# Kernel optimization log

Measured on AMD Instinct MI355X. Metric: run time of the kernel, lower is better.

Reference implementation:

```python
import jax, jax.numpy as jnp
import numpy as np

N = 32768      # total nodes = 256 graphs x 128 nodes
G = 256        # graphs in batch
NPG = 128      # nodes per graph
DEG = 8        # incoming edges per node
E = N * DEG    # 262144 edges
F_IN = 64      # node feature size
F_E = 16       # edge feature size
EMB = 64       # out_channels per head == embedding_size
H = 4          # attention heads
HC = H * EMB   # 256
DENSE = 256
K = 64         # ceil(0.5 * NPG)
EPS = 1e-5


def setup_inputs() -> dict:
    key = jax.random.key(0)
    ks = list(jax.random.split(key, 32))
    it = iter(ks)
    s = 0.05

    def rn(shape):
        return jax.random.normal(next(it), shape, jnp.float32) * s

    x = jax.random.normal(next(it), (N, F_IN), jnp.float32)
    dst = jnp.repeat(jnp.arange(N, dtype=jnp.int32), DEG)
    src = (dst // NPG) * NPG + jax.random.randint(next(it), (E,), 0, NPG, dtype=jnp.int32)
    edge_index = jnp.stack([src, dst])                      # [2, E], edges stay within graph
    edge_attr = jax.random.normal(next(it), (E, F_E), jnp.float32)
    batch_index = jnp.arange(N, dtype=jnp.int32) // NPG

    inp = dict(
        x=x, edge_index=edge_index, edge_attr=edge_attr, batch_index=batch_index,
        # TransformerConv 1 (in=F_IN)
        Wq1=rn((F_IN, HC)), bq1=jnp.zeros((HC,), jnp.float32),
        Wk1=rn((F_IN, HC)), bk1=jnp.zeros((HC,), jnp.float32),
        Wv1=rn((F_IN, HC)), bv1=jnp.zeros((HC,), jnp.float32),
        We1=rn((F_E, HC)),
        Ws1=rn((F_IN, HC)), bs1=jnp.zeros((HC,), jnp.float32),
        Wb1=rn((3 * HC, 1)),
        t1_W=rn((HC, EMB)), t1_b=jnp.zeros((EMB,), jnp.float32),
        bn1_g=jnp.ones((EMB,), jnp.float32), bn1_b=jnp.zeros((EMB,), jnp.float32),
        # TransformerConv 2 (in=EMB)
        Wq2=rn((EMB, HC)), bq2=jnp.zeros((HC,), jnp.float32),
        Wk2=rn((EMB, HC)), bk2=jnp.zeros((HC,), jnp.float32),
        Wv2=rn((EMB, HC)), bv2=jnp.zeros((HC,), jnp.float32),
        We2=rn((F_E, HC)),
        Ws2=rn((EMB, HC)), bs2=jnp.zeros((HC,), jnp.float32),
        Wb2=rn((3 * HC, 1)),
        t2_W=rn((HC, EMB)), t2_b=jnp.zeros((EMB,), jnp.float32),
        bn2_g=jnp.ones((EMB,), jnp.float32), bn2_b=jnp.zeros((EMB,), jnp.float32),
        # TopKPooling + MLP head
        pool_w=rn((EMB,)),
        l1_W=rn((2 * EMB, DENSE)), l1_b=jnp.zeros((DENSE,), jnp.float32),
        l2_W=rn((DENSE, DENSE // 2)), l2_b=jnp.zeros((DENSE // 2,), jnp.float32),
        l3_W=rn((DENSE // 2, 1)), l3_b=jnp.zeros((1,), jnp.float32),
    )
    return inp


def _tconv(x, src, dst, ea, Wq, bq, Wk, bk, Wv, bv, We, Ws, bs, Wb):
    """PyG TransformerConv with edge_dim, beta=True, concat=True."""
    n = x.shape[0]
    q = (x @ Wq + bq).reshape(n, H, EMB)                    # [N,H,C]
    eemb = (ea @ We).reshape(-1, H, EMB)                    # [E,H,C]
    k = (x @ Wk + bk)[src].reshape(-1, H, EMB) + eemb       # edge features added to key
    v = (x @ Wv + bv)[src].reshape(-1, H, EMB) + eemb       # and to value
    alpha = jnp.einsum('ehc,ehc->eh', q[dst], k) / jnp.sqrt(jnp.float32(EMB))  # [E,H]
    # stable segment softmax over incoming edges of each dst node
    amax = jax.ops.segment_max(alpha, dst, num_segments=n)
    pexp = jnp.exp(alpha - amax[dst])
    denom = jax.ops.segment_sum(pexp, dst, num_segments=n)
    attn = pexp / denom[dst]                                # [E,H]
    out = jax.ops.segment_sum(v * attn[..., None], dst, num_segments=n).reshape(n, HC)
    # beta gated skip: lin_skip(x) and lin_beta([out, xr, out-xr])
    xr = x @ Ws + bs
    beta = jax.nn.sigmoid(jnp.concatenate([out, xr, out - xr], axis=-1) @ Wb)  # [N,1]
    return beta * xr + (1.0 - beta) * out


def _bn(x, g, b):
    m = x.mean(0)
    v = x.var(0)
    return g * (x - m) * jax.lax.rsqrt(v + EPS) + b


def _forward(x, edge_attr,
             Wq1, bq1, Wk1, bk1, Wv1, bv1, We1, Ws1, bs1, Wb1, t1_W, t1_b, bn1_g, bn1_b,
             Wq2, bq2, Wk2, bk2, Wv2, bv2, We2, Ws2, bs2, Wb2, t2_W, t2_b, bn2_g, bn2_b,
             pool_w, l1_W, l1_b, l2_W, l2_b, l3_W, l3_b,
             edge_index, batch_index):
    src, dst = edge_index[0], edge_index[1]
    h = _tconv(x, src, dst, edge_attr, Wq1, bq1, Wk1, bk1, Wv1, bv1, We1, Ws1, bs1, Wb1)
    h = _bn(jax.nn.relu(h @ t1_W + t1_b), bn1_g, bn1_b)
    h = _tconv(h, src, dst, edge_attr, Wq2, bq2, Wk2, bk2, Wv2, bv2, We2, Ws2, bs2, Wb2)
    h = _bn(jax.nn.relu(h @ t2_W + t2_b), bn2_g, bn2_b)
    # TopKPooling: score = (x.w)/||w||, keep top K per graph, scale by tanh(score)
    score = (h @ pool_w) / jnp.linalg.norm(pool_w)          # [N]
    sv, si = jax.lax.top_k(score.reshape(G, NPG), K)        # [G,K]
    xs = jnp.take_along_axis(h.reshape(G, NPG, EMB), si[..., None], axis=1)  # [G,K,EMB]
    xs = xs * jnp.tanh(sv)[..., None]
    # readout: global max pool || global mean pool
    rep = jnp.concatenate([xs.max(axis=1), xs.mean(axis=1)], axis=-1)  # [G, 2*EMB]
    hd = jax.nn.relu(rep @ l1_W + l1_b)
    hd = jax.nn.relu(hd @ l2_W + l2_b)
    return hd @ l3_W + l3_b                                  # [G,1]


def reference(x, edge_index, edge_attr, batch_index,
              Wq1, bq1, Wk1, bk1, Wv1, bv1, We1, Ws1, bs1, Wb1, t1_W, t1_b, bn1_g, bn1_b,
              Wq2, bq2, Wk2, bk2, Wv2, bv2, We2, Ws2, bs2, Wb2, t2_W, t2_b, bn2_g, bn2_b,
              pool_w, l1_W, l1_b, l2_W, l2_b, l3_W, l3_b):
    return _forward(x, edge_attr,
                    Wq1, bq1, Wk1, bk1, Wv1, bv1, We1, Ws1, bs1, Wb1, t1_W, t1_b, bn1_g, bn1_b,
                    Wq2, bq2, Wk2, bk2, Wv2, bv2, We2, Ws2, bs2, Wb2, t2_W, t2_b, bn2_g, bn2_b,
                    pool_w, l1_W, l1_b, l2_W, l2_b, l3_W, l3_b,
                    edge_index, batch_index)
```

## Files before the change

### kernel.cpp

```cpp
#include <hip/hip_runtime.h>
#include <math.h>

#define NN 32768
#define NG 256
#define DEG 8
#define HC 256
#define NCAT 1088
#define HCP 320
#define KTOP 64
#define EPSBN 1e-5f

typedef __attribute__((ext_vector_type(8))) short short8v;
typedef __attribute__((ext_vector_type(4))) float f32x4;

__device__ inline float bf2f(unsigned short u) {
    union { unsigned int i; float f; } c; c.i = ((unsigned int)u) << 16; return c.f;
}
__device__ inline unsigned short f2bf(float f) {
    union { float f; unsigned int i; } c; c.f = f;
    unsigned int r = c.i + 0x7FFFu + ((c.i >> 16) & 1u);
    return (unsigned short)(r >> 16);
}
__device__ inline void split2(float v, unsigned short& hi, unsigned short& lo) {
    hi = f2bf(v);
    lo = f2bf(v - bf2f(hi));
}

__global__ __launch_bounds__(256) void split_x(
    const float* __restrict__ X,
    unsigned short* __restrict__ Xhi, unsigned short* __restrict__ Xlo)
{
    size_t i8 = ((size_t)blockIdx.x * 256 + threadIdx.x) * 8;
    float4 a0 = *(const float4*)(X + i8);
    float4 a1 = *(const float4*)(X + i8 + 4);
    float av[8] = {a0.x, a0.y, a0.z, a0.w, a1.x, a1.y, a1.z, a1.w};
    short8v vh, vl;
    #pragma unroll
    for (int j = 0; j < 8; j++) {
        unsigned short h, l;
        split2(av[j], h, l);
        vh[j] = (short)h; vl[j] = (short)l;
    }
    *(short8v*)(Xhi + i8) = vh;
    *(short8v*)(Xlo + i8) = vl;
}

__global__ __launch_bounds__(256) void prep(
    const float* __restrict__ Wq, const float* __restrict__ bq,
    const float* __restrict__ Wk, const float* __restrict__ bk,
    const float* __restrict__ Wv, const float* __restrict__ bv,
    const float* __restrict__ Ws, const float* __restrict__ bs,
    const float* __restrict__ We, const float* __restrict__ tW,
    const float* __restrict__ Wb,
    unsigned short* __restrict__ WThi, unsigned short* __restrict__ WTlo,
    float* __restrict__ bcat,
    unsigned short* __restrict__ tWThi, unsigned short* __restrict__ tWTlo,
    float* __restrict__ Wbf, float* __restrict__ stats)
{
    const int t = threadIdx.x, b = blockIdx.x;
    if (b < 16) {
        int n = b * 64 + (t >> 2);
        int cc = n & 255;
        const float* src = (n < 256) ? Wq : (n < 512) ? Wk : (n < 768) ? Wv : Ws;
        int k0 = (t & 3) * 16;
        #pragma unroll
        for (int k = k0; k < k0 + 16; k++) {
            unsigned short h, l;
            split2(src[k * 256 + cc], h, l);
            WThi[n * 64 + k] = h; WTlo[n * 64 + k] = l;
        }
    } else if (b < 32) {
        int idx = (b - 16) * 256 + t;
        int k = idx >> 6, o = idx & 63;
        int h = o >> 4, f = o & 15;
        const float* wq = Wq + k * 256 + h * 64;
        const float* we = We + f * 256 + h * 64;
        float s = 0.f;
        #pragma unroll
        for (int d = 0; d < 64; d++) s += wq[d] * we[d];
        unsigned short hh, ll;
        split2(s, hh, ll);
        WThi[(1024 + o) * 64 + k] = hh; WTlo[(1024 + o) * 64 + k] = ll;
    } else if (b < 48) {
        int idx = (b - 32) * 256 + t;
        int kp = idx >> 6, n = idx & 63;
        int h = kp >> 4, f = kp & 15;
        const float* we = We + f * 256 + h * 64;
        const float* tw = tW + (h * 64) * 64 + n;
        float s = 0.f;
        #pragma unroll
        for (int d = 0; d < 64; d++) s += we[d] * tw[d * 64];
        unsigned short hh, ll;
        split2(s, hh, ll);
        tWThi[n * HCP + 256 + kp] = hh; tWTlo[n * HCP + 256 + kp] = ll;
    } else if (b < 64) {
        int base = (b - 48) * 1024 + t * 4;
        #pragma unroll
        for (int i = 0; i < 4; i++) {
            int idx = base + i;
            int n = idx >> 8, k = idx & 255;
            unsigned short h, l;
            split2(tW[k * 64 + n], h, l);
            tWThi[n * HCP + k] = h; tWTlo[n * HCP + k] = l;
        }
    } else {
        if (t < 128) stats[t] = 0.f;
        Wbf[t]       = Wb[t]       + Wb[512 + t];
        Wbf[256 + t] = Wb[256 + t] - Wb[512 + t];
        for (int c = t; c < 1024; c += 256) {
            int cc = c & 255;
            bcat[c] = (c < 256) ? bq[cc] : (c < 512) ? bk[cc] : (c < 768) ? bv[cc] : bs[cc];
        }
        if (t < 64) {
            int h = t >> 4, f = t & 15;
            const float* we = We + f * 256 + h * 64;
            float s = 0.f, sb = 0.f;
            #pragma unroll
            for (int d = 0; d < 64; d++) {
                s  += we[d] * (Wb[h * 64 + d] + Wb[512 + h * 64 + d]);
                sb += we[d] * bq[h * 64 + d];
            }
            Wbf[512 + t] = s;
            bcat[1024 + t] = sb;
        }
    }
}

__global__ __launch_bounds__(256) void proj_mfma(
    const unsigned short* __restrict__ Ahi, const unsigned short* __restrict__ Alo,
    const unsigned short* __restrict__ WThi, const unsigned short* __restrict__ WTlo,
    const float* __restrict__ bcat, unsigned short* __restrict__ C)
{
    __shared__ char smem[32768];
    unsigned short* AhiL = (unsigned short*)smem;
    unsigned short* AloL = AhiL + 4096;
    unsigned short* WhiL = AloL + 4096;
    unsigned short* WloL = WhiL + 4096;
    float* CL = (float*)smem;
    const int t = threadIdx.x;
    const int n0 = blockIdx.x * 64;
    const int row0 = blockIdx.y * 64;

    #pragma unroll
    for (int g = 0; g < 2; g++) {
        int idx = t * 8 + g * 2048;
        int r = idx >> 6, c = idx & 63;
        int ch = (c >> 3) ^ (r & 7);
        *(short8v*)(AhiL + r * 64 + ch * 8) =
            *(const short8v*)(Ahi + (size_t)(row0 + r) * 64 + c);
        *(short8v*)(AloL + r * 64 + ch * 8) =
            *(const short8v*)(Alo + (size_t)(row0 + r) * 64 + c);
        *(short8v*)(WhiL + r * 64 + ch * 8) =
            *(const short8v*)(WThi + (size_t)(n0 + r) * 64 + c);
        *(short8v*)(WloL + r * 64 + ch * 8) =
            *(const short8v*)(WTlo + (size_t)(n0 + r) * 64 + c);
    }
    __syncthreads();

    const int w = t >> 6, l = t & 63;
    const int lr = l & 15, lg = l >> 4, ls = l & 7;
    f32x4 acc[4] = {};
    #pragma unroll
    for (int kk = 0; kk < 2; kk++) {
        int ch = (kk * 4 + lg) ^ ls;
        short8v ah = *(short8v*)(AhiL + (w * 16 + lr) * 64 + ch * 8);
        short8v al = *(short8v*)(AloL + (w * 16 + lr) * 64 + ch * 8);
        #pragma unroll
        for (int nt = 0; nt < 4; nt++) {
            short8v bh = *(short8v*)(WhiL + (nt * 16 + lr) * 64 + ch * 8);
            short8v bl = *(short8v*)(WloL + (nt * 16 + lr) * 64 + ch * 8);
            acc[nt] = __builtin_amdgcn_mfma_f32_16x16x32_bf16(ah, bh, acc[nt], 0, 0, 0);
            acc[nt] = __builtin_amdgcn_mfma_f32_16x16x32_bf16(al, bh, acc[nt], 0, 0, 0);
            acc[nt] = __builtin_amdgcn_mfma_f32_16x16x32_bf16(ah, bl, acc[nt], 0, 0, 0);
        }
    }
    __syncthreads();
    #pragma unroll
    for (int nt = 0; nt < 4; nt++)
        #pragma unroll
        for (int r = 0; r < 4; r++)
            CL[(w * 16 + lg * 4 + r) * 68 + nt * 16 + lr] = acc[nt][r];
    __syncthreads();
    {
        int r = t >> 2, cb = (t & 3) * 16;
        #pragma unroll
        for (int jj = 0; jj < 2; jj++) {
            f32x4 p0 = *(f32x4*)(CL + r * 68 + cb + jj * 8);
            f32x4 p1 = *(f32x4*)(CL + r * 68 + cb + jj * 8 + 4);
            float4 b0 = *(const float4*)(bcat + n0 + cb + jj * 8);
            float4 b1 = *(const float4*)(bcat + n0 + cb + jj * 8 + 4);
            short8v o;
            o[0] = (short)f2bf(p0[0] + b0.x); o[1] = (short)f2bf(p0[1] + b0.y);
            o[2] = (short)f2bf(p0[2] + b0.z); o[3] = (short)f2bf(p0[3] + b0.w);
            o[4] = (short)f2bf(p1[0] + b1.x); o[5] = (short)f2bf(p1[1] + b1.y);
            o[6] = (short)f2bf(p1[2] + b1.z); o[7] = (short)f2bf(p1[3] + b1.w);
            *(short8v*)(C + (size_t)(row0 + r) * NCAT + n0 + cb + jj * 8) = o;
        }
    }
}

__global__ __launch_bounds__(256) void gemm_t(
    const unsigned short* __restrict__ Ahi, const unsigned short* __restrict__ Alo,
    const unsigned short* __restrict__ WThi, const unsigned short* __restrict__ WTlo,
    const float* __restrict__ bias, float* __restrict__ Tout,
    float* __restrict__ stats)
{
    __shared__ char smem[32768];
    unsigned short* AhiL = (unsigned short*)smem;
    unsigned short* AloL = AhiL + 4096;
    unsigned short* WhiL = AloL + 4096;
    unsigned short* WloL = WhiL + 4096;
    float* CL = (float*)smem;
    const int t = threadIdx.x;
    const int row0 = blockIdx.x * 64;
    const int w = t >> 6, l = t & 63;
    const int lr = l & 15, lg = l >> 4, ls = l & 7;
    f32x4 acc[4] = {};
    for (int kt = 0; kt < 5; kt++) {
        if (kt) __syncthreads();
        #pragma unroll
        for (int g = 0; g < 2; g++) {
            int idx = t * 8 + g * 2048;
            int r = idx >> 6, c = idx & 63;
            int ch = (c >> 3) ^ (r & 7);
            *(short8v*)(AhiL + r * 64 + ch * 8) =
                *(const short8v*)(Ahi + (size_t)(row0 + r) * HCP + kt * 64 + c);
            *(short8v*)(AloL + r * 64 + ch * 8) =
                *(const short8v*)(Alo + (size_t)(row0 + r) * HCP + kt * 64 + c);
            *(short8v*)(WhiL + r * 64 + ch * 8) =
                *(const short8v*)(WThi + r * HCP + kt * 64 + c);
            *(short8v*)(WloL + r * 64 + ch * 8) =
                *(const short8v*)(WTlo + r * HCP + kt * 64 + c);
        }
        __syncthreads();
        #pragma unroll
        for (int kk = 0; kk < 2; kk++) {
            int ch = (kk * 4 + lg) ^ ls;
            short8v ah = *(short8v*)(AhiL + (w * 16 + lr) * 64 + ch * 8);
            short8v al = *(short8v*)(AloL + (w * 16 + lr) * 64 + ch * 8);
            #pragma unroll
            for (int nt = 0; nt < 4; nt++) {
                short8v bh = *(short8v*)(WhiL + (nt * 16 + lr) * 64 + ch * 8);
                short8v bl = *(short8v*)(WloL + (nt * 16 + lr) * 64 + ch * 8);
                acc[nt] = __builtin_amdgcn_mfma_f32_16x16x32_bf16(ah, bh, acc[nt], 0, 0, 0);
                acc[nt] = __builtin_amdgcn_mfma_f32_16x16x32_bf16(al, bh, acc[nt], 0, 0, 0);
                acc[nt] = __builtin_amdgcn_mfma_f32_16x16x32_bf16(ah, bl, acc[nt], 0, 0, 0);
            }
        }
    }
    __syncthreads();
    #pragma unroll
    for (int nt = 0; nt < 4; nt++)
        #pragma unroll
        for (int r = 0; r < 4; r++)
            CL[(w * 16 + lg * 4 + r) * 68 + nt * 16 + lr] = acc[nt][r];
    __syncthreads();
    {
        int r = t >> 2, cb = (t & 3) * 16;
        #pragma unroll
        for (int jj = 0; jj < 4; jj++) {
            f32x4 p = *(f32x4*)(CL + r * 68 + cb + jj * 4);
            float4 bb = *(const float4*)(bias + cb + jj * 4);
            float4 o;
            o.x = fmaxf(p[0] + bb.x, 0.f); o.y = fmaxf(p[1] + bb.y, 0.f);
            o.z = fmaxf(p[2] + bb.z, 0.f); o.w = fmaxf(p[3] + bb.w, 0.f);
            *(float4*)(Tout + (size_t)(row0 + r) * 64 + cb + jj * 4) = o;
        }
    }
    if (t < 64) {
        float bb = bias[t];
        float s = 0.f, s2 = 0.f;
        #pragma unroll 8
        for (int r = 0; r < 64; r++) {
            float v = fmaxf(CL[r * 68 + t] + bb, 0.f);
            s += v; s2 += v * v;
        }
        atomicAdd(&stats[t], s);
        atomicAdd(&stats[64 + t], s2);
    }
}

__global__ __launch_bounds__(256) void attn_fused(
    const unsigned short* __restrict__ C,
    const float* __restrict__ Wbf,
    const int* __restrict__ srcIdx, const float* __restrict__ EA,
    unsigned short* __restrict__ Hhi, unsigned short* __restrict__ Hlo)
{
    const int t = threadIdx.x;
    const int lane = t & 63;
    const int bid = blockIdx.x;
    const int swz = (bid & 7) * 512 + (bid >> 3);
    const int n = swz * 8 + (t >> 5);
    const int l = lane & 31;
    const int c0 = l * 8;
    const int h = l >> 3;
    const int fl = l & 7;
    const int gb = lane & 56;

    const unsigned short* rowN = C + (size_t)n * NCAT;
    short8v qv = *(const short8v*)(rowN + c0);
    float q[8];
    #pragma unroll
    for (int i = 0; i < 8; i++) q[i] = bf2f((unsigned short)qv[i]);
    float qe0 = bf2f(rowN[1024 + h * 16 + 2 * fl]);
    float qe1 = bf2f(rowN[1024 + h * 16 + 2 * fl + 1]);

    const int ebase = n * DEG;
    int sj = srcIdx[ebase + fl];
    int ss[DEG];
    #pragma unroll
    for (int j = 0; j < DEG; j++) ss[j] = __shfl(sj, gb | j);

    short8v kv[DEG];
    float2 eav[DEG];
    #pragma unroll
    for (int j = 0; j < DEG; j++) {
        kv[j] = *(const short8v*)(C + (size_t)ss[j] * NCAT + 256 + c0);
        eav[j] = *(const float2*)(EA + (size_t)(ebase + j) * 16 + 2 * fl);
    }
    float alpha[DEG];
    #pragma unroll
    for (int j = 0; j < DEG; j++) {
        float d = eav[j].x * qe0 + eav[j].y * qe1;
        #pragma unroll
        for (int i = 0; i < 8; i++) d += q[i] * bf2f((unsigned short)kv[j][i]);
        alpha[j] = d;
    }
    #pragma unroll
    for (int j = 0; j < DEG; j++) {
        float d = alpha[j];
        d += __shfl_xor(d, 1); d += __shfl_xor(d, 2); d += __shfl_xor(d, 4);
        alpha[j] = d * 0.125f;
    }
    float mx = alpha[0];
    #pragma unroll
    for (int j = 1; j < DEG; j++) mx = fmaxf(mx, alpha[j]);
    float wsum = 0.f, wgt[DEG];
    #pragma unroll
    for (int j = 0; j < DEG; j++) { wgt[j] = expf(alpha[j] - mx); wsum += wgt[j]; }
    float inv = 1.f / wsum;

    float o[8] = {};
    float eg0 = 0.f, eg1 = 0.f;
    #pragma unroll
    for (int j = 0; j < DEG; j++) {
        float wj = wgt[j] * inv;
        eg0 += wj * eav[j].x; eg1 += wj * eav[j].y;
        short8v vv = *(const short8v*)(C + (size_t)ss[j] * NCAT + 512 + c0);
        #pragma unroll
        for (int i = 0; i < 8; i++) o[i] += wj * bf2f((unsigned short)vv[i]);
    }

    short8v sv = *(const short8v*)(rowN + 768 + c0);
    float xr[8];
    #pragma unroll
    for (int i = 0; i < 8; i++) xr[i] = bf2f((unsigned short)sv[i]);

    float2 we13 = *(const float2*)(Wbf + 512 + l * 2);
    float part = eg0 * we13.x + eg1 * we13.y;
    {
        f32x4 w13a = *(const f32x4*)(Wbf + c0);
        f32x4 w13b = *(const f32x4*)(Wbf + c0 + 4);
        f32x4 w23a = *(const f32x4*)(Wbf + 256 + c0);
        f32x4 w23b = *(const f32x4*)(Wbf + 256 + c0 + 4);
        #pragma unroll
        for (int i = 0; i < 4; i++) {
            part += o[i] * w13a[i] + xr[i] * w23a[i];
            part += o[4 + i] * w13b[i] + xr[4 + i] * w23b[i];
        }
    }
    part += __shfl_xor(part, 1);  part += __shfl_xor(part, 2);
    part += __shfl_xor(part, 4);  part += __shfl_xor(part, 8);
    part += __shfl_xor(part, 16);
    float beta = 1.f / (1.f + expf(-part));
    float omb = 1.f - beta;

    short8v hh, hl;
    #pragma unroll
    for (int i = 0; i < 8; i++) {
        float hv = beta * xr[i] + omb * o[i];
        unsigned short a, b;
        split2(hv, a, b);
        hh[i] = (short)a; hl[i] = (short)b;
    }
    *(short8v*)(Hhi + (size_t)n * HCP + c0) = hh;
    *(short8v*)(Hlo + (size_t)n * HCP + c0) = hl;

    ushort2 zh, zl;
    split2(omb * eg0, zh.x, zl.x);
    split2(omb * eg1, zh.y, zl.y);
    *(ushort2*)(Hhi + (size_t)n * HCP + 256 + l * 2) = zh;
    *(ushort2*)(Hlo + (size_t)n * HCP + 256 + l * 2) = zl;
}

__global__ __launch_bounds__(256) void bn_apply(
    float* __restrict__ T, const float* __restrict__ stats,
    const float* __restrict__ g, const float* __restrict__ b,
    unsigned short* __restrict__ Thi, unsigned short* __restrict__ Tlo)
{
    int i = blockIdx.x * 256 + threadIdx.x;
    int c = i & 63;
    float mean = stats[c] * (1.f / NN);
    float var  = stats[64 + c] * (1.f / NN) - mean * mean;
    float v = T[i];
    float r = g[c] * (v - mean) * rsqrtf(var + EPSBN) + b[c];
    T[i] = r;
    unsigned short h, l;
    split2(r, h, l);
    Thi[i] = h; Tlo[i] = l;
}

__global__ __launch_bounds__(128) void pool_mlp(
    const float* __restrict__ Hn, const float* __restrict__ pw,
    const float* __restrict__ W1, const float* __restrict__ b1,
    const float* __restrict__ W2, const float* __restrict__ b2,
    const float* __restrict__ W3, const float* __restrict__ b3,
    float* __restrict__ out)
{
    __shared__ float sh[128][65];
    __shared__ float spw[64];
    __shared__ float sc[128];
    __shared__ float sscale[128];
    __shared__ int   skeep[128];
    __shared__ float rmax[2][64], rsum[2][64];
    __shared__ float srep[128];
    __shared__ float sh1[256];
    __shared__ float sh2[128];
    __shared__ float wred[2];
    const int g = blockIdx.x, t = threadIdx.x;

    for (int i = t; i < 128 * 64; i += 128) sh[i >> 6][i & 63] = Hn[(size_t)g * 128 * 64 + i];
    if (t < 64) spw[t] = pw[t];
    __syncthreads();

    float nw = 0.f;
    #pragma unroll
    for (int i = 0; i < 64; i++) { float w = spw[i]; nw += w * w; }
    float invn = rsqrtf(nw);

    float s = 0.f;
    #pragma unroll
    for (int i = 0; i < 64; i++) s += sh[t][i] * spw[i];
    s *= invn;
    sc[t] = s;
    __syncthreads();

    int rank = 0;
    for (int m = 0; m < 128; m++) {
        float sm = sc[m];
        rank += (sm > s) || (sm == s && m < t);
    }
    skeep[t] = (rank < KTOP);
    sscale[t] = tanhf(s);
    __syncthreads();

    {
        int c = t & 63, half = t >> 6;
        float mxv = -1e30f, sm = 0.f;
        for (int r = half * 64; r < half * 64 + 64; r++) {
            if (skeep[r]) {
                float v = sh[r][c] * sscale[r];
                mxv = fmaxf(mxv, v); sm += v;
            }
        }
        rmax[half][c] = mxv; rsum[half][c] = sm;
    }
    __syncthreads();
    if (t < 64) {
        srep[t] = fmaxf(rmax[0][t], rmax[1][t]);
        srep[64 + t] = (rsum[0][t] + rsum[1][t]) * (1.f / KTOP);
    }
    __syncthreads();

    #pragma unroll
    for (int jj = 0; jj < 2; jj++) {
        int j = t + jj * 128;
        float a = b1[j];
        for (int c2 = 0; c2 < 128; c2++) a += srep[c2] * W1[c2 * 256 + j];
        sh1[j] = fmaxf(a, 0.f);
    }
    __syncthreads();
    {
        float a = b2[t];
        for (int c2 = 0; c2 < 256; c2++) a += sh1[c2] * W2[c2 * 128 + t];
        sh2[t] = fmaxf(a, 0.f);
    }
    __syncthreads();
    float p = sh2[t] * W3[t];
    p += __shfl_xor(p, 1);  p += __shfl_xor(p, 2);  p += __shfl_xor(p, 4);
    p += __shfl_xor(p, 8);  p += __shfl_xor(p, 16); p += __shfl_xor(p, 32);
    if ((t & 63) == 0) wred[t >> 6] = p;
    __syncthreads();
    if (t == 0) out[g] = wred[0] + wred[1] + b3[0];
}

extern "C" void kernel_launch(void* const* d_in, const int* in_sizes, int n_in,
                              void* d_out, int out_size, void* d_ws, size_t ws_size,
                              hipStream_t stream)
{
    const float* x    = (const float*)d_in[0];
    const int*   ei   = (const int*)  d_in[1];
    const float* ea   = (const float*)d_in[2];
    const int*   srcI = ei;
    const float* Wq1 = (const float*)d_in[4];  const float* bq1 = (const float*)d_in[5];
    const float* Wk1 = (const float*)d_in[6];  const float* bk1 = (const float*)d_in[7];
    const float* Wv1 = (const float*)d_in[8];  const float* bv1 = (const float*)d_in[9];
    const float* We1 = (const float*)d_in[10];
    const float* Ws1 = (const float*)d_in[11]; const float* bs1 = (const float*)d_in[12];
    const float* Wb1 = (const float*)d_in[13];
    const float* t1W = (const float*)d_in[14]; const float* t1b = (const float*)d_in[15];
    const float* g1  = (const float*)d_in[16]; const float* be1 = (const float*)d_in[17];
    const float* Wq2 = (const float*)d_in[18]; const float* bq2 = (const float*)d_in[19];
    const float* Wk2 = (const float*)d_in[20]; const float* bk2 = (const float*)d_in[21];
    const float* Wv2 = (const float*)d_in[22]; const float* bv2 = (const float*)d_in[23];
    const float* We2 = (const float*)d_in[24];
    const float* Ws2 = (const float*)d_in[25]; const float* bs2 = (const float*)d_in[26];
    const float* Wb2 = (const float*)d_in[27];
    const float* t2W = (const float*)d_in[28]; const float* t2b = (const float*)d_in[29];
    const float* g2  = (const float*)d_in[30]; const float* be2 = (const float*)d_in[31];
    const float* pw  = (const float*)d_in[32];
    const float* l1W = (const float*)d_in[33]; const float* l1b = (const float*)d_in[34];
    const float* l2W = (const float*)d_in[35]; const float* l2b = (const float*)d_in[36];
    const float* l3W = (const float*)d_in[37]; const float* l3b = (const float*)d_in[38];

    char* ws = (char*)d_ws;
    unsigned short* C   = (unsigned short*)ws;
    unsigned short* Hhi = (unsigned short*)(ws + (size_t)NN * NCAT * 2);
    unsigned short* Hlo = Hhi + (size_t)NN * HCP;
    float* bT    = (float*)(Hlo + (size_t)NN * HCP);
    unsigned short* bThi = (unsigned short*)(bT + (size_t)NN * 64);
    unsigned short* bTlo = bThi + (size_t)NN * 64;
    unsigned short* Xhi  = bTlo + (size_t)NN * 64;
    unsigned short* Xlo  = Xhi + (size_t)NN * 64;
    float* bcat  = (float*)(Xlo + (size_t)NN * 64);
    float* stats = bcat + NCAT;
    float* Wbf   = stats + 128;
    unsigned short* WThi  = (unsigned short*)(Wbf + 576);
    unsigned short* WTlo  = WThi + (size_t)NCAT * 64;
    unsigned short* tWThi = WTlo + (size_t)NCAT * 64;
    unsigned short* tWTlo = tWThi + 64 * HCP;

    const dim3 blk(256);
    const dim3 gProj(17, 512);

    split_x<<<NN * 64 / (256 * 8), blk, 0, stream>>>(x, Xhi, Xlo);
    prep<<<65, blk, 0, stream>>>(Wq1, bq1, Wk1, bk1, Wv1, bv1, Ws1, bs1, We1, t1W, Wb1,
                                 WThi, WTlo, bcat, tWThi, tWTlo, Wbf, stats);
    proj_mfma<<<gProj, blk, 0, stream>>>(Xhi, Xlo, WThi, WTlo, bcat, C);
    attn_fused<<<NN / 8, blk, 0, stream>>>(C, Wbf, srcI, ea, Hhi, Hlo);
    gemm_t<<<512, blk, 0, stream>>>(Hhi, Hlo, tWThi, tWTlo, t1b, bT, stats);
    bn_apply<<<NN * 64 / 256, blk, 0, stream>>>(bT, stats, g1, be1, bThi, bTlo);

    prep<<<65, blk, 0, stream>>>(Wq2, bq2, Wk2, bk2, Wv2, bv2, Ws2, bs2, We2, t2W, Wb2,
                                 WThi, WTlo, bcat, tWThi, tWTlo, Wbf, stats);
    proj_mfma<<<gProj, blk, 0, stream>>>(bThi, bTlo, WThi, WTlo, bcat, C);
    attn_fused<<<NN / 8, blk, 0, stream>>>(C, Wbf, srcI, ea, Hhi, Hlo);
    gemm_t<<<512, blk, 0, stream>>>(Hhi, Hlo, tWThi, tWTlo, t2b, bT, stats);
    bn_apply<<<NN * 64 / 256, blk, 0, stream>>>(bT, stats, g2, be2, bThi, bTlo);

    pool_mlp<<<NG, 128, 0, stream>>>(bT, pw, l1W, l1b, l2W, l2b, l3W, l3b,
                                     (float*)d_out);
}
```

Baseline: 225.4 us.

## Map one wavefront per node in attention and skip unused fp32 BN store

The attention kernel now assigns a full 64-lane wavefront to each destination node instead of half a wavefront. Each lane handles 4 channels and one edge-feature element, and the launch grid doubles. This lowers per-thread register pressure and adds an occupancy hint, with the aim of hiding more gather latency, at the cost of narrower 8-byte loads and an extra shuffle stage. Separately, the first batch-norm pass no longer writes its fp32 output, which only the second pass feeds to pooling, saving one full-tensor store.

```diff
diff --git a/kernel.cpp b/kernel.cpp
--- a/kernel.cpp
+++ b/kernel.cpp
@@ -280,7 +280,7 @@
     }
 }
 
-__global__ __launch_bounds__(256) void attn_fused(
+__global__ __launch_bounds__(256, 8) void attn_fused(
     const unsigned short* __restrict__ C,
     const float* __restrict__ Wbf,
     const int* __restrict__ srcIdx, const float* __restrict__ EA,
@@ -288,115 +288,95 @@
 {
     const int t = threadIdx.x;
     const int lane = t & 63;
+    const int wave = t >> 6;
     const int bid = blockIdx.x;
-    const int swz = (bid & 7) * 512 + (bid >> 3);
-    const int n = swz * 8 + (t >> 5);
-    const int l = lane & 31;
-    const int c0 = l * 8;
-    const int h = l >> 3;
-    const int fl = l & 7;
-    const int gb = lane & 56;
+    const int swz = (bid & 7) * 1024 + (bid >> 3);
+    const int n = swz * 4 + wave;
+    const int c0 = lane * 4;
+    const int h = lane >> 4;
+    const int fi = lane & 15;
 
     const unsigned short* rowN = C + (size_t)n * NCAT;
-    short8v qv = *(const short8v*)(rowN + c0);
-    float q[8];
-    #pragma unroll
-    for (int i = 0; i < 8; i++) q[i] = bf2f((unsigned short)qv[i]);
-    float qe0 = bf2f(rowN[1024 + h * 16 + 2 * fl]);
-    float qe1 = bf2f(rowN[1024 + h * 16 + 2 * fl + 1]);
+    ushort4 qv = *(const ushort4*)(rowN + c0);
+    float q0 = bf2f(qv.x), q1 = bf2f(qv.y), q2 = bf2f(qv.z), q3 = bf2f(qv.w);
+    float qe_l = bf2f(rowN[1024 + h * 16 + fi]);
 
     const int ebase = n * DEG;
-    int sj = srcIdx[ebase + fl];
+    int sj = srcIdx[ebase + (lane & 7)];
     int ss[DEG];
     #pragma unroll
-    for (int j = 0; j < DEG; j++) ss[j] = __shfl(sj, gb | j);
-
-    short8v kv[DEG];
-    float2 eav[DEG];
+    for (int j = 0; j < DEG; j++) ss[j] = __shfl(sj, j);
+
+    ushort4 kv[DEG];
+    float eav[DEG];
     #pragma unroll
     for (int j = 0; j < DEG; j++) {
-        kv[j] = *(const short8v*)(C + (size_t)ss[j] * NCAT + 256 + c0);
-        eav[j] = *(const float2*)(EA + (size_t)(ebase + j) * 16 + 2 * fl);
+        kv[j] = *(const ushort4*)(C + (size_t)ss[j] * NCAT + 256 + c0);
+        eav[j] = EA[(size_t)(ebase + j) * 16 + fi];
     }
     float alpha[DEG];
     #pragma unroll
     for (int j = 0; j < DEG; j++) {
-        float d = eav[j].x * qe0 + eav[j].y * qe1;
-        #pragma unroll
-        for (int i = 0; i < 8; i++) d += q[i] * bf2f((unsigned short)kv[j][i]);
-        alpha[j] = d;
-    }
+        float d = eav[j] * qe_l
+                + q0 * bf2f(kv[j].x) + q1 * bf2f(kv[j].y)
+                + q2 * bf2f(kv[j].z) + q3 * bf2f(kv[j].w);
+        d += __shfl_xor(d, 1); d += __shfl_xor(d, 2);
+        d += __shfl_xor(d, 4); d += __shfl_xor(d, 8);
+        alpha[j] = d * 0.125f;
+    }
+    float mx = alpha[0];
+    #pragma unroll
+    for (int j = 1; j < DEG; j++) mx = fmaxf(mx, alpha[j]);
+    float wsum = 0.f;
+    #pragma unroll
+    for (int j = 0; j < DEG; j++) { alpha[j] = expf(alpha[j] - mx); wsum += alpha[j]; }
+    float inv = 1.f / wsum;
+
+    float o0 = 0.f, o1 = 0.f, o2 = 0.f, o3 = 0.f, eg = 0.f;
     #pragma unroll
     for (int j = 0; j < DEG; j++) {
-        float d = alpha[j];
-        d += __shfl_xor(d, 1); d += __shfl_xor(d, 2); d += __shfl_xor(d, 4);
-        alpha[j] = d * 0.125f;
-    }
-    float mx = alpha[0];
-    #pragma unroll
-    for (int j = 1; j < DEG; j++) mx = fmaxf(mx, alpha[j]);
-    float wsum = 0.f, wgt[DEG];
-    #pragma unroll
-    for (int j = 0; j < DEG; j++) { wgt[j] = expf(alpha[j] - mx); wsum += wgt[j]; }
-    float inv = 1.f / wsum;
-
-    float o[8] = {};
-    float eg0 = 0.f, eg1 = 0.f;
-    #pragma unroll
-    for (int j = 0; j < DEG; j++) {
-        float wj = wgt[j] * inv;
-        eg0 += wj * eav[j].x; eg1 += wj * eav[j].y;
-        short8v vv = *(const short8v*)(C + (size_t)ss[j] * NCAT + 512 + c0);
-        #pragma unroll
-        for (int i = 0; i < 8; i++) o[i] += wj * bf2f((unsigned short)vv[i]);
-    }
-
-    short8v sv = *(const short8v*)(rowN + 768 + c0);
-    float xr[8];
-    #pragma unroll
-    for (int i = 0; i < 8; i++) xr[i] = bf2f((unsigned short)sv[i]);
-
-    float2 we13 = *(const float2*)(Wbf + 512 + l * 2);
-    float part = eg0 * we13.x + eg1 * we13.y;
+        float wj = alpha[j] * inv;
+        eg += wj * eav[j];
+        ushort4 vv = *(const ushort4*)(C + (size_t)ss[j] * NCAT + 512 + c0);
+        o0 += wj * bf2f(vv.x); o1 += wj * bf2f(vv.y);
+        o2 += wj * bf2f(vv.z); o3 += wj * bf2f(vv.w);
+    }
+
+    ushort4 sv = *(const ushort4*)(rowN + 768 + c0);
+    float xr0 = bf2f(sv.x), xr1 = bf2f(sv.y), xr2 = bf2f(sv.z), xr3 = bf2f(sv.w);
+
+    float part = eg * Wbf[512 + lane];
     {
-        f32x4 w13a = *(const f32x4*)(Wbf + c0);
-        f32x4 w13b = *(const f32x4*)(Wbf + c0 + 4);
-        f32x4 w23a = *(const f32x4*)(Wbf + 256 + c0);
-        f32x4 w23b = *(const f32x4*)(Wbf + 256 + c0 + 4);
-        #pragma unroll
-        for (int i = 0; i < 4; i++) {
-            part += o[i] * w13a[i] + xr[i] * w23a[i];
-            part += o[4 + i] * w13b[i] + xr[4 + i] * w23b[i];
-        }
+        f32x4 w13 = *(const f32x4*)(Wbf + c0);
+        f32x4 w23 = *(const f32x4*)(Wbf + 256 + c0);
+        part += o0 * w13[0] + o1 * w13[1] + o2 * w13[2] + o3 * w13[3];
+        part += xr0 * w23[0] + xr1 * w23[1] + xr2 * w23[2] + xr3 * w23[3];
     }
     part += __shfl_xor(part, 1);  part += __shfl_xor(part, 2);
     part += __shfl_xor(part, 4);  part += __shfl_xor(part, 8);
-    part += __shfl_xor(part, 16);
+    part += __shfl_xor(part, 16); part += __shfl_xor(part, 32);
     float beta = 1.f / (1.f + expf(-part));
     float omb = 1.f - beta;
 
-    short8v hh, hl;
-    #pragma unroll
-    for (int i = 0; i < 8; i++) {
-        float hv = beta * xr[i] + omb * o[i];
-        unsigned short a, b;
-        split2(hv, a, b);
-        hh[i] = (short)a; hl[i] = (short)b;
-    }
-    *(short8v*)(Hhi + (size_t)n * HCP + c0) = hh;
-    *(short8v*)(Hlo + (size_t)n * HCP + c0) = hl;
-
-    ushort2 zh, zl;
-    split2(omb * eg0, zh.x, zl.x);
-    split2(omb * eg1, zh.y, zl.y);
-    *(ushort2*)(Hhi + (size_t)n * HCP + 256 + l * 2) = zh;
-    *(ushort2*)(Hlo + (size_t)n * HCP + 256 + l * 2) = zl;
+    ushort4 hh, hl;
+    split2(beta * xr0 + omb * o0, hh.x, hl.x);
+    split2(beta * xr1 + omb * o1, hh.y, hl.y);
+    split2(beta * xr2 + omb * o2, hh.z, hl.z);
+    split2(beta * xr3 + omb * o3, hh.w, hl.w);
+    *(ushort4*)(Hhi + (size_t)n * HCP + c0) = hh;
+    *(ushort4*)(Hlo + (size_t)n * HCP + c0) = hl;
+
+    unsigned short zh, zl;
+    split2(omb * eg, zh, zl);
+    Hhi[(size_t)n * HCP + 256 + lane] = zh;
+    Hlo[(size_t)n * HCP + 256 + lane] = zl;
 }
 
 __global__ __launch_bounds__(256) void bn_apply(
     float* __restrict__ T, const float* __restrict__ stats,
     const float* __restrict__ g, const float* __restrict__ b,
-    unsigned short* __restrict__ Thi, unsigned short* __restrict__ Tlo)
+    unsigned short* __restrict__ Thi, unsigned short* __restrict__ Tlo,
+    int wf32)
 {
     int i = blockIdx.x * 256 + threadIdx.x;
     int c = i & 63;
@@ -404,7 +384,7 @@
     float var  = stats[64 + c] * (1.f / NN) - mean * mean;
     float v = T[i];
     float r = g[c] * (v - mean) * rsqrtf(var + EPSBN) + b[c];
-    T[i] = r;
+    if (wf32) T[i] = r;
     unsigned short h, l;
     split2(r, h, l);
     Thi[i] = h; Tlo[i] = l;
@@ -547,16 +527,16 @@
     prep<<<65, blk, 0, stream>>>(Wq1, bq1, Wk1, bk1, Wv1, bv1, Ws1, bs1, We1, t1W, Wb1,
                                  WThi, WTlo, bcat, tWThi, tWTlo, Wbf, stats);
     proj_mfma<<<gProj, blk, 0, stream>>>(Xhi, Xlo, WThi, WTlo, bcat, C);
-    attn_fused<<<NN / 8, blk, 0, stream>>>(C, Wbf, srcI, ea, Hhi, Hlo);
+    attn_fused<<<NN / 4, blk, 0, stream>>>(C, Wbf, srcI, ea, Hhi, Hlo);
     gemm_t<<<512, blk, 0, stream>>>(Hhi, Hlo, tWThi, tWTlo, t1b, bT, stats);
-    bn_apply<<<NN * 64 / 256, blk, 0, stream>>>(bT, stats, g1, be1, bThi, bTlo);
+    bn_apply<<<NN * 64 / 256, blk, 0, stream>>>(bT, stats, g1, be1, bThi, bTlo, 0);
 
     prep<<<65, blk, 0, stream>>>(Wq2, bq2, Wk2, bk2, Wv2, bv2, Ws2, bs2, We2, t2W, Wb2,
                                  WThi, WTlo, bcat, tWThi, tWTlo, Wbf, stats);
     proj_mfma<<<gProj, blk, 0, stream>>>(bThi, bTlo, WThi, WTlo, bcat, C);
-    attn_fused<<<NN / 8, blk, 0, stream>>>(C, Wbf, srcI, ea, Hhi, Hlo);
+    attn_fused<<<NN / 4, blk, 0, stream>>>(C, Wbf, srcI, ea, Hhi, Hlo);
     gemm_t<<<512, blk, 0, stream>>>(Hhi, Hlo, tWThi, tWTlo, t2b, bT, stats);
-    bn_apply<<<NN * 64 / 256, blk, 0, stream>>>(bT, stats, g2, be2, bThi, bTlo);
+    bn_apply<<<NN * 64 / 256, blk, 0, stream>>>(bT, stats, g2, be2, bThi, bTlo, 1);
 
     pool_mlp<<<NG, 128, 0, stream>>>(bT, pw, l1W, l1b, l2W, l2b, l3W, l3b,
                                      (float*)d_out);
```

After: 220.1 us. -2.3%, faster.
